# Kernel tuning notes

Measured on AMD Instinct MI355X. Metric: run time of the kernel, lower is better.

Reference implementation:

```python
import jax, jax.numpy as jnp
import numpy as np

M, K, N = 4096, 7168, 18432  # tokens, in_features, out_features


def setup_inputs() -> dict:
    key = jax.random.key(0)
    kx, kw, ks = jax.random.split(key, 3)
    x = jax.random.normal(kx, (M, K), dtype=jnp.float32)
    # int8 quantized weight, layout [in_features, out_features] as in the torch module
    weight = jax.random.randint(kw, (K, N), -128, 128, dtype=jnp.int8)
    # per-output-channel dequant scale (bf16 in the original; fp32 here for a stable baseline)
    scale = jax.random.uniform(ks, (N,), dtype=jnp.float32) * 0.02 + 1e-3
    return {"x": x, "weight": weight, "scale": scale}


def reference(x, weight, scale):
    # Fused dequant + GEMM: y = x @ (int8_weight * scale_per_out_channel)
    w = weight.astype(x.dtype) * scale.astype(x.dtype)[None, :]  # [K, N]
    return x @ w  # [M, N]
```

## Files before the change

### kernel.cpp

```cpp
#include <hip/hip_runtime.h>
#include <hip/hip_bf16.h>
#include <cstdint>
#include <cstddef>

#define M_ 4096
#define K_ 7168
#define N_ 18432
#define NT 56
#define ITERS 28

typedef __attribute__((ext_vector_type(4))) int i32x4;

#define AS1 __attribute__((address_space(1)))
#define AS3 __attribute__((address_space(3)))

__device__ __forceinline__ void gld_lds16(void* lds, const void* g) {
  __builtin_amdgcn_global_load_lds((const AS1 void*)g, (AS3 void*)lds, 16, 0, 0);
}

__global__ __launch_bounds__(256) void quant_x_kernel(const float* __restrict__ x,
                                                      signed char* __restrict__ xq,
                                                      float* __restrict__ sx) {
  const int m = blockIdx.x;
  const float4* row4 = (const float4*)(x + (size_t)m * K_);
  float mx = 0.f;
  for (int i = threadIdx.x; i < K_ / 4; i += 256) {
    float4 v = row4[i];
    mx = fmaxf(mx, fmaxf(fmaxf(fabsf(v.x), fabsf(v.y)), fmaxf(fabsf(v.z), fabsf(v.w))));
  }
#pragma unroll
  for (int d = 1; d < 64; d <<= 1) mx = fmaxf(mx, __shfl_xor(mx, d));
  __shared__ float wred[4];
  if ((threadIdx.x & 63) == 0) wred[threadIdx.x >> 6] = mx;
  __syncthreads();
  mx = fmaxf(fmaxf(wred[0], wred[1]), fmaxf(wred[2], wred[3]));
  const float inv = mx > 0.f ? 127.f / mx : 0.f;
  if (threadIdx.x == 0) sx[m] = mx / 127.f;
  char4* q4 = (char4*)(xq + (size_t)m * K_);
  for (int i = threadIdx.x; i < K_ / 4; i += 256) {
    float4 v = row4[i];
    char4 c;
    c.x = (signed char)__float2int_rn(v.x * inv);
    c.y = (signed char)__float2int_rn(v.y * inv);
    c.z = (signed char)__float2int_rn(v.z * inv);
    c.w = (signed char)__float2int_rn(v.w * inv);
    q4[i] = c;
  }
}

__global__ __launch_bounds__(256) void transpose_w_kernel(const int* __restrict__ W,
                                                          signed char* __restrict__ Wt) {
  __shared__ __align__(16) signed char t[64][80];
  const int k0 = blockIdx.x * 64;
  const int n0 = blockIdx.y * 64;
  const int r = threadIdx.x >> 4;
  const int c4 = (threadIdx.x & 15) * 4;
#pragma unroll
  for (int rr = 0; rr < 4; ++rr) {
    const int row = rr * 16 + r;
    int4 v = *(const int4*)(W + (size_t)(k0 + row) * N_ + n0 + c4);
    t[c4 + 0][row] = (signed char)v.x;
    t[c4 + 1][row] = (signed char)v.y;
    t[c4 + 2][row] = (signed char)v.z;
    t[c4 + 3][row] = (signed char)v.w;
  }
  __syncthreads();
  const int nr = threadIdx.x >> 2;
  const int cb = (threadIdx.x & 3) * 16;
  int4 o = *(const int4*)&t[nr][cb];
  *(int4*)(Wt + (size_t)(n0 + nr) * K_ + k0 + cb) = o;
}

__global__ __launch_bounds__(512, 2) void gemm_i8_kernel(const signed char* __restrict__ Aq,
                                                         const signed char* __restrict__ Bt,
                                                         const float* __restrict__ sx,
                                                         const float* __restrict__ scale,
                                                         float* __restrict__ C) {
  __shared__ __align__(16) signed char lds[131072];

  const int bid = blockIdx.x;
  const int xcd = bid & 7;
  const int j = bid >> 3;
  const int m0 = (j & 15) * 256;
  const int n0 = (xcd * 9 + (j >> 4)) * 256;

  const int tid = threadIdx.x;
  const int w = tid >> 6;
  const int lane = tid & 63;
  const int wr = w >> 2;
  const int wc = w & 3;

  const int fr = lane & 15;
  const int q = lane >> 4;
  const int sl = ((q ^ ((fr >> 1) & 3)) << 4);

  const int ls16 = (((lane & 3) ^ ((lane >> 3) & 3)) << 4);
  const int pr0 = w * 16 + (lane >> 2);
  const unsigned offA0 = (unsigned)(m0 + pr0) * K_ + ls16;
  const unsigned offA1 = (unsigned)(m0 + 128 + pr0) * K_ + ls16;
  const unsigned offB0 = (unsigned)(n0 + pr0) * K_ + ls16;
  const unsigned offB1 = (unsigned)(n0 + 128 + pr0) * K_ + ls16;

#define STAGE_A(T, KS) do {                                                        \
    const int tc_ = (T) < NT ? (T) : NT - 1;                                       \
    signed char* d_ = lds + (((T) & 1) * 32768 + (KS) * 16384 + w * 1024);         \
    gld_lds16(d_, Aq + (size_t)offA0 + tc_ * 128 + (KS) * 64);                     \
    gld_lds16(d_ + 8192, Aq + (size_t)offA1 + tc_ * 128 + (KS) * 64);              \
  } while (0)
#define STAGE_B(T, KS) do {                                                        \
    const int tc_ = (T) < NT ? (T) : NT - 1;                                       \
    signed char* d_ = lds + (65536 + ((T) & 1) * 32768 + (KS) * 16384 + w * 1024); \
    gld_lds16(d_, Bt + (size_t)offB0 + tc_ * 128 + (KS) * 64);                     \
    gld_lds16(d_ + 8192, Bt + (size_t)offB1 + tc_ * 128 + (KS) * 64);              \
  } while (0)
#define LDA_TO(DST, BUF, KS, MH) do {                                              \
    const signed char* ab = lds + ((BUF) * 32768 + (KS) * 16384);                  \
    _Pragma("unroll") for (int i_ = 0; i_ < 4; ++i_)                               \
      DST[i_] = *(const i32x4*)(ab + (wr * 128 + ((MH) * 4 + i_) * 16 + fr) * 64 + sl); \
  } while (0)
#define LDB_TO(DST, BUF, KS) do {                                                  \
    const signed char* bb = lds + (65536 + (BUF) * 32768 + (KS) * 16384);          \
    _Pragma("unroll") for (int n_ = 0; n_ < 4; ++n_)                               \
      DST[n_] = *(const i32x4*)(bb + (wc * 64 + n_ * 16 + fr) * 64 + sl);          \
  } while (0)
#define MFMA16(MH, AQ, BQ) do {                                                    \
    __builtin_amdgcn_s_setprio(1);                                                 \
    _Pragma("unroll") for (int i_ = 0; i_ < 4; ++i_)                               \
    _Pragma("unroll") for (int n_ = 0; n_ < 4; ++n_)                               \
      acc[(MH) * 4 + i_][n_] = __builtin_amdgcn_mfma_i32_16x16x64_i8(              \
          AQ[i_], BQ[n_], acc[(MH) * 4 + i_][n_], 0, 0, 0);                        \
    __builtin_amdgcn_s_setprio(0);                                                 \
  } while (0)
#define FENCE asm volatile("" ::: "memory")
#define BAR do { FENCE; __builtin_amdgcn_s_barrier(); FENCE; } while (0)
#define VM6 do { asm volatile("s_waitcnt vmcnt(6)" ::: "memory"); \
                 __builtin_amdgcn_sched_barrier(0); } while (0)
#define SB __builtin_amdgcn_sched_barrier(0)

  i32x4 acc[8][4] = {};
  i32x4 aq0[4], aq1[4], bq0[4], bq1[4];

  STAGE_B(0, 0); STAGE_A(0, 0); STAGE_B(0, 1); STAGE_A(0, 1);
  STAGE_B(1, 0); STAGE_A(1, 0); STAGE_B(1, 1);
  VM6;
  BAR;
  LDB_TO(bq0, 0, 0); LDA_TO(aq0, 0, 0, 0);
  SB;

  for (int it = 0; it < ITERS; ++it) {
    const int u = 2 * it;
    STAGE_A(u + 1, 1);
    BAR;
    LDA_TO(aq1, 0, 0, 1);
    SB;
    MFMA16(0, aq0, bq0);
    BAR;
    STAGE_B(u + 2, 0);
    BAR;
    LDB_TO(bq1, 0, 1); LDA_TO(aq0, 0, 1, 0);
    SB;
    MFMA16(1, aq1, bq0);
    BAR;
    STAGE_A(u + 2, 0);
    BAR;
    LDA_TO(aq1, 0, 1, 1);
    SB;
    MFMA16(0, aq0, bq1);
    BAR;
    STAGE_B(u + 2, 1);
    BAR;
    VM6;
    LDB_TO(bq0, 1, 0); LDA_TO(aq0, 1, 0, 0);
    SB;
    MFMA16(1, aq1, bq1);
    BAR;
    STAGE_A(u + 2, 1);
    BAR;
    LDA_TO(aq1, 1, 0, 1);
    SB;
    MFMA16(0, aq0, bq0);
    BAR;
    STAGE_B(u + 3, 0);
    BAR;
    LDB_TO(bq1, 1, 1); LDA_TO(aq0, 1, 1, 0);
    SB;
    MFMA16(1, aq1, bq0);
    BAR;
    STAGE_A(u + 3, 0);
    BAR;
    LDA_TO(aq1, 1, 1, 1);
    SB;
    MFMA16(0, aq0, bq1);
    BAR;
    STAGE_B(u + 3, 1);
    BAR;
    VM6;
    LDB_TO(bq0, 0, 0); LDA_TO(aq0, 0, 0, 0);
    SB;
    MFMA16(1, aq1, bq1);
    BAR;
  }

  const int mb = m0 + wr * 128;
  const int nb = n0 + wc * 64;
  const int col = lane & 15;
  const int rq = (lane >> 4) * 4;
  float scl[4];
#pragma unroll
  for (int n = 0; n < 4; ++n) scl[n] = scale[nb + n * 16 + col];
#pragma unroll
  for (int m = 0; m < 8; ++m) {
#pragma unroll
    for (int r = 0; r < 4; ++r) {
      const int row = mb + m * 16 + rq + r;
      const float s = sx[row];
      float* out = C + (size_t)row * N_ + nb + col;
#pragma unroll
      for (int n = 0; n < 4; ++n) out[n * 16] = (float)acc[m][n][r] * s * scl[n];
    }
  }
#undef STAGE_A
#undef STAGE_B
#undef LDA_TO
#undef LDB_TO
#undef MFMA16
#undef FENCE
#undef BAR
#undef VM6
#undef SB
}

__global__ __launch_bounds__(256) void fb_gemm_kernel(const float* __restrict__ X,
                                                      const int* __restrict__ W,
                                                      const float* __restrict__ scale,
                                                      float* __restrict__ Y) {
  __shared__ float xs[16][65];
  __shared__ float ws_[16][65];
  const int bn = blockIdx.x * 64;
  const int bm = blockIdx.y * 64;
  const int tx = threadIdx.x & 15;
  const int ty = threadIdx.x >> 4;
  float acc[4][4] = {};
  for (int k0 = 0; k0 < K_; k0 += 16) {
    for (int i = threadIdx.x; i < 64 * 16; i += 256) {
      int r = i >> 4, c = i & 15;
      xs[c][r] = X[(size_t)(bm + r) * K_ + k0 + c];
    }
    for (int i = threadIdx.x; i < 16 * 64; i += 256) {
      int r = i >> 6, c = i & 63;
      ws_[r][c] = (float)W[(size_t)(k0 + r) * N_ + bn + c];
    }
    __syncthreads();
#pragma unroll
    for (int kk = 0; kk < 16; ++kk) {
      float a[4], b[4];
#pragma unroll
      for (int i = 0; i < 4; ++i) a[i] = xs[kk][ty * 4 + i];
#pragma unroll
      for (int j = 0; j < 4; ++j) b[j] = ws_[kk][tx * 4 + j];
#pragma unroll
      for (int i = 0; i < 4; ++i)
#pragma unroll
        for (int j = 0; j < 4; ++j) acc[i][j] += a[i] * b[j];
    }
    __syncthreads();
  }
#pragma unroll
  for (int i = 0; i < 4; ++i)
#pragma unroll
    for (int j = 0; j < 4; ++j)
      Y[(size_t)(bm + ty * 4 + i) * N_ + bn + tx * 4 + j] = acc[i][j] * scale[bn + tx * 4 + j];
}

extern "C" void kernel_launch(void* const* d_in, const int* in_sizes, int n_in,
                              void* d_out, int out_size, void* d_ws, size_t ws_size,
                              hipStream_t stream) {
  const float* x = (const float*)d_in[0];
  const int* w = (const int*)d_in[1];
  const float* scale = (const float*)d_in[2];
  float* y = (float*)d_out;

  const size_t xq_bytes = (size_t)M_ * K_;
  const size_t sx_off = xq_bytes;
  const size_t wt_off = sx_off + (size_t)M_ * 4;
  const size_t need = wt_off + (size_t)N_ * K_;

  if (ws_size >= need) {
    signed char* xq = (signed char*)d_ws;
    float* sx = (float*)((char*)d_ws + sx_off);
    signed char* wt = (signed char*)((char*)d_ws + wt_off);
    hipLaunchKernelGGL(quant_x_kernel, dim3(M_), dim3(256), 0, stream, x, xq, sx);
    hipLaunchKernelGGL(transpose_w_kernel, dim3(K_ / 64, N_ / 64), dim3(256), 0, stream, w, wt);
    hipLaunchKernelGGL(gemm_i8_kernel, dim3((M_ / 256) * (N_ / 256)), dim3(512), 0, stream,
                       xq, wt, sx, scale, y);
  } else {
    hipLaunchKernelGGL(fb_gemm_kernel, dim3(N_ / 64, M_ / 64), dim3(256), 0, stream,
                       x, w, scale, y);
  }
}
```

Baseline: 725.2 us.

## Restructure int8 GEMM main loop into coarse ping-pong phases with fewer barriers

Replaces the fine-grained schedule, which interleaved half-tile LDS reads and 16-MFMA groups with a barrier around every step, with four phases per iteration. Each phase loads a full k-slice of A (8 fragments) and B (4 fragments) from LDS, issues 32 MFMAs, and stages the next A and B slices together. The aim is to cut barrier count and scheduling stalls and to give each wave longer MFMA bursts that hide global-to-LDS loads. In exchange it needs more fragment registers, and the vmcnt waits are changed to match the new load ordering.

```diff
diff --git a/kernel.cpp b/kernel.cpp
--- a/kernel.cpp
+++ b/kernel.cpp
@@ -113,91 +113,65 @@
     gld_lds16(d_, Bt + (size_t)offB0 + tc_ * 128 + (KS) * 64);                     \
     gld_lds16(d_ + 8192, Bt + (size_t)offB1 + tc_ * 128 + (KS) * 64);              \
   } while (0)
-#define LDA_TO(DST, BUF, KS, MH) do {                                              \
+#define LDALL(FA, FB, BUF, KS) do {                                                \
     const signed char* ab = lds + ((BUF) * 32768 + (KS) * 16384);                  \
-    _Pragma("unroll") for (int i_ = 0; i_ < 4; ++i_)                               \
-      DST[i_] = *(const i32x4*)(ab + (wr * 128 + ((MH) * 4 + i_) * 16 + fr) * 64 + sl); \
-  } while (0)
-#define LDB_TO(DST, BUF, KS) do {                                                  \
     const signed char* bb = lds + (65536 + (BUF) * 32768 + (KS) * 16384);          \
+    _Pragma("unroll") for (int f_ = 0; f_ < 8; ++f_)                               \
+      FA[f_] = *(const i32x4*)(ab + (wr * 128 + f_ * 16 + fr) * 64 + sl);          \
     _Pragma("unroll") for (int n_ = 0; n_ < 4; ++n_)                               \
-      DST[n_] = *(const i32x4*)(bb + (wc * 64 + n_ * 16 + fr) * 64 + sl);          \
-  } while (0)
-#define MFMA16(MH, AQ, BQ) do {                                                    \
+      FB[n_] = *(const i32x4*)(bb + (wc * 64 + n_ * 16 + fr) * 64 + sl);           \
+  } while (0)
+#define MFMA32(FA, FB) do {                                                        \
     __builtin_amdgcn_s_setprio(1);                                                 \
-    _Pragma("unroll") for (int i_ = 0; i_ < 4; ++i_)                               \
+    _Pragma("unroll") for (int f_ = 0; f_ < 8; ++f_)                               \
     _Pragma("unroll") for (int n_ = 0; n_ < 4; ++n_)                               \
-      acc[(MH) * 4 + i_][n_] = __builtin_amdgcn_mfma_i32_16x16x64_i8(              \
-          AQ[i_], BQ[n_], acc[(MH) * 4 + i_][n_], 0, 0, 0);                        \
+      acc[f_][n_] = __builtin_amdgcn_mfma_i32_16x16x64_i8(                         \
+          FA[f_], FB[n_], acc[f_][n_], 0, 0, 0);                                   \
     __builtin_amdgcn_s_setprio(0);                                                 \
   } while (0)
 #define FENCE asm volatile("" ::: "memory")
 #define BAR do { FENCE; __builtin_amdgcn_s_barrier(); FENCE; } while (0)
-#define VM6 do { asm volatile("s_waitcnt vmcnt(6)" ::: "memory"); \
-                 __builtin_amdgcn_sched_barrier(0); } while (0)
+#define VM4 asm volatile("s_waitcnt vmcnt(4)" ::: "memory")
+#define VM8 asm volatile("s_waitcnt vmcnt(8)" ::: "memory")
 #define SB __builtin_amdgcn_sched_barrier(0)
 
   i32x4 acc[8][4] = {};
-  i32x4 aq0[4], aq1[4], bq0[4], bq1[4];
-
-  STAGE_B(0, 0); STAGE_A(0, 0); STAGE_B(0, 1); STAGE_A(0, 1);
-  STAGE_B(1, 0); STAGE_A(1, 0); STAGE_B(1, 1);
-  VM6;
+  i32x4 frA0[8], frB0[4], frA1[8], frB1[4];
+
+  STAGE_A(0, 0); STAGE_B(0, 0); STAGE_A(0, 1); STAGE_B(0, 1);
+  STAGE_A(1, 0); STAGE_B(1, 0); STAGE_A(1, 1); STAGE_B(1, 1);
+  VM8;
   BAR;
-  LDB_TO(bq0, 0, 0); LDA_TO(aq0, 0, 0, 0);
+  LDALL(frA0, frB0, 0, 0);
   SB;
 
   for (int it = 0; it < ITERS; ++it) {
     const int u = 2 * it;
-    STAGE_A(u + 1, 1);
-    BAR;
-    LDA_TO(aq1, 0, 0, 1);
-    SB;
-    MFMA16(0, aq0, bq0);
-    BAR;
-    STAGE_B(u + 2, 0);
-    BAR;
-    LDB_TO(bq1, 0, 1); LDA_TO(aq0, 0, 1, 0);
-    SB;
-    MFMA16(1, aq1, bq0);
-    BAR;
-    STAGE_A(u + 2, 0);
-    BAR;
-    LDA_TO(aq1, 0, 1, 1);
-    SB;
-    MFMA16(0, aq0, bq1);
-    BAR;
-    STAGE_B(u + 2, 1);
-    BAR;
-    VM6;
-    LDB_TO(bq0, 1, 0); LDA_TO(aq0, 1, 0, 0);
-    SB;
-    MFMA16(1, aq1, bq1);
-    BAR;
-    STAGE_A(u + 2, 1);
-    BAR;
-    LDA_TO(aq1, 1, 0, 1);
-    SB;
-    MFMA16(0, aq0, bq0);
-    BAR;
-    STAGE_B(u + 3, 0);
-    BAR;
-    LDB_TO(bq1, 1, 1); LDA_TO(aq0, 1, 1, 0);
-    SB;
-    MFMA16(1, aq1, bq0);
-    BAR;
-    STAGE_A(u + 3, 0);
-    BAR;
-    LDA_TO(aq1, 1, 1, 1);
-    SB;
-    MFMA16(0, aq0, bq1);
-    BAR;
-    STAGE_B(u + 3, 1);
-    BAR;
-    VM6;
-    LDB_TO(bq0, 0, 0); LDA_TO(aq0, 0, 0, 0);
-    SB;
-    MFMA16(1, aq1, bq1);
+    LDALL(frA1, frB1, 0, 1);
+    SB;
+    MFMA32(frA0, frB0);
+    SB;
+    STAGE_A(u + 2, 0); STAGE_B(u + 2, 0);
+    VM4;
+    BAR;
+    LDALL(frA0, frB0, 1, 0);
+    SB;
+    MFMA32(frA1, frB1);
+    SB;
+    STAGE_A(u + 2, 1); STAGE_B(u + 2, 1);
+    BAR;
+    LDALL(frA1, frB1, 1, 1);
+    SB;
+    MFMA32(frA0, frB0);
+    SB;
+    STAGE_A(u + 3, 0); STAGE_B(u + 3, 0);
+    VM4;
+    BAR;
+    LDALL(frA0, frB0, 0, 0);
+    SB;
+    MFMA32(frA1, frB1);
+    SB;
+    STAGE_A(u + 3, 1); STAGE_B(u + 3, 1);
     BAR;
   }
 
@@ -221,12 +195,12 @@
   }
 #undef STAGE_A
 #undef STAGE_B
-#undef LDA_TO
-#undef LDB_TO
-#undef MFMA16
+#undef LDALL
+#undef MFMA32
 #undef FENCE
 #undef BAR
-#undef VM6
+#undef VM4
+#undef VM8
 #undef SB
 }
 
```

After: 1.249 ms. 72.3% more time.
